# Kernel optimization log

Hardware: AMD Instinct MI355X
Metric: run time of the kernel (lower is better)

Reference implementation:

```python
import jax, jax.numpy as jnp
import numpy as np

B, P, C, D, H = 32, 2048, 19, 512, 4
DH = D // H  # 128
EPS = 1e-5


def setup_inputs() -> dict:
    key = jax.random.key(0)
    ks = jax.random.split(key, 12)
    s = 0.02
    return {
        "x": jax.random.normal(ks[0], (B, P, D), jnp.float32),
        "channel_embeddings": jax.random.normal(ks[1], (C, D), jnp.float32),
        "Wq": jax.random.normal(ks[2], (D, D), jnp.float32) * s,
        "bq": jnp.zeros((D,), jnp.float32),
        "Wk": jax.random.normal(ks[3], (D, D), jnp.float32) * s,
        "bk": jnp.zeros((D,), jnp.float32),
        "Wv": jax.random.normal(ks[4], (D, D), jnp.float32) * s,
        "bv": jnp.zeros((D,), jnp.float32),
        "Wo": jax.random.normal(ks[5], (D, D), jnp.float32) * s,
        "bo": jnp.zeros((D,), jnp.float32),
        "gamma": jnp.ones((D,), jnp.float32),
        "beta": jnp.zeros((D,), jnp.float32),
    }


def reference(x, channel_embeddings, Wq, bq, Wk, bk, Wv, bv, Wo, bo, gamma, beta):
    # q: (B, P, H, DH)
    q = (x @ Wq.T + bq).reshape(B, P, H, DH)
    # K/V depend only on channel embeddings (same for every batch/patch in the
    # original; it merely materialized the broadcast). Compute once: (C, H, DH)
    k = (channel_embeddings @ Wk.T + bk).reshape(C, H, DH)
    v = (channel_embeddings @ Wv.T + bv).reshape(C, H, DH)
    # scores over channels: (B, P, C, H)
    scores = jnp.einsum("bphd,chd->bpch", q, k) / jnp.sqrt(jnp.float32(DH))
    weights = jax.nn.softmax(scores, axis=2)  # softmax over channel dim
    # weighted sum of channel values: (B, P, H, DH) -> (B, P, D)
    attended = jnp.einsum("bpch,chd->bphd", weights, v).reshape(B, P, D)
    out = attended @ Wo.T + bo  # dropout is identity in eval mode
    # residual + layernorm
    h = x + out
    mean = jnp.mean(h, axis=-1, keepdims=True)
    var = jnp.mean(jnp.square(h - mean), axis=-1, keepdims=True)
    return (h - mean) * jax.lax.rsqrt(var + EPS) * gamma + beta
```

## Files before the change

### kernel.cpp

```cpp
#include <hip/hip_runtime.h>
#include <hip/hip_bf16.h>

#define B_  32
#define P_  2048
#define C_  19
#define D_  512
#define H_  4
#define DH_ 128
#define NROW (B_*P_)
#define CHP_ 96

typedef float f32x4 __attribute__((ext_vector_type(4)));
typedef short bf16x8 __attribute__((ext_vector_type(8)));
typedef unsigned short ushort4v __attribute__((ext_vector_type(4)));

__device__ __forceinline__ unsigned short f2bf(float f) {
  union { __hip_bfloat16 h; unsigned short s; } u;
  u.h = __float2bfloat16(f);
  return u.s;
}

__device__ __forceinline__ bf16x8 ld_cvt8(const float* p) {
  f32x4 v0 = *(const f32x4*)p;
  f32x4 v1 = *(const f32x4*)(p + 4);
  bf16x8 a;
  a[0]=(short)f2bf(v0[0]); a[1]=(short)f2bf(v0[1]);
  a[2]=(short)f2bf(v0[2]); a[3]=(short)f2bf(v0[3]);
  a[4]=(short)f2bf(v1[0]); a[5]=(short)f2bf(v1[1]);
  a[6]=(short)f2bf(v1[2]); a[7]=(short)f2bf(v1[3]);
  return a;
}

__global__ __launch_bounds__(256) void prep1(
    const float* __restrict__ ce,
    const float* __restrict__ Wk, const float* __restrict__ bk,
    const float* __restrict__ Wv, const float* __restrict__ bv,
    float* __restrict__ Kg, float* __restrict__ Vg)
{
  int g = blockIdx.x * 256 + threadIdx.x;
  if (g >= 2*C_*D_) return;
  int which = (g >= C_*D_) ? 1 : 0;
  int idx = which ? (g - C_*D_) : g;
  int c = idx >> 9;
  int n = idx & (D_-1);
  const float* w = (which ? Wv : Wk) + (size_t)n * D_;
  const float* e = ce + (size_t)c * D_;
  float s = 0.f;
  #pragma unroll 8
  for (int d = 0; d < D_; ++d) s = fmaf(e[d], w[d], s);
  s += (which ? bv : bk)[n];
  if (which) Vg[idx] = s; else Kg[idx] = s;
}

__global__ __launch_bounds__(512) void prep2(
    const float* __restrict__ Wq, const float* __restrict__ bq,
    const float* __restrict__ Wo,
    const float* __restrict__ Kg, const float* __restrict__ Vg,
    unsigned short* __restrict__ Mtf, unsigned short* __restrict__ Utf,
    float* __restrict__ s0g)
{
  int p = blockIdx.x;
  int m = threadIdx.x;

  const int mt_off = (p>>4)*8192 + (m>>5)*512 + ((((m>>3)&3)<<4) + (p&15))*8 + (m&7);
  const int ut_off = ((m>>4)*3 + (p>>5))*512 + ((((p>>3)&3)<<4) + (m&15))*8 + (p&7);

  int c = p >> 2, h = p & 3;
  if (c >= C_) {
    if (p < 80) { Mtf[mt_off] = 0; if (m == 0) s0g[p] = 0.f; }
    Utf[ut_off] = 0;
    return;
  }
  const float rs128 = 0.08838834764831843f;
  const float* Kr = Kg + c*D_ + h*DH_;
  const float* Vr = Vg + c*D_ + h*DH_;

  float macc = 0.f;
  #pragma unroll 4
  for (int dh = 0; dh < DH_; ++dh)
    macc = fmaf(Wq[(size_t)(h*DH_+dh)*D_ + m], Kr[dh], macc);
  Mtf[mt_off] = f2bf(macc * rs128);

  float uacc = 0.f;
  const float* wor = Wo + (size_t)m*D_ + h*DH_;
  #pragma unroll 4
  for (int dh = 0; dh < DH_; ++dh)
    uacc = fmaf(wor[dh], Vr[dh], uacc);
  Utf[ut_off] = f2bf(uacc);

  if (m == 0) {
    float sa = 0.f;
    const float* bqr = bq + h*DH_;
    for (int dh = 0; dh < DH_; ++dh) sa = fmaf(bqr[dh], Kr[dh], sa);
    s0g[p] = sa * rs128;
  }
}

__global__ __launch_bounds__(256) void fused64(
    const float* __restrict__ x,
    const unsigned short* __restrict__ Mtf,
    const unsigned short* __restrict__ Utf,
    const float* __restrict__ s0g,
    const float* __restrict__ bo,
    const float* __restrict__ gamma, const float* __restrict__ beta,
    float* __restrict__ out)
{
  __shared__ __attribute__((aligned(16))) unsigned short WaL[64][104];
  __shared__ float rs_[64][2], rq_[64][2];

  const int t    = threadIdx.x;
  const int wave = t >> 6;
  const int lane = t & 63;
  const int lhi  = lane >> 4;
  const int llo  = lane & 15;
  const int row0 = blockIdx.x * 64;

  {
    const int wrow = wave * 16;
    f32x4 acc0 = (f32x4){0,0,0,0}, acc1 = acc0, acc2 = acc0, acc3 = acc0, acc4 = acc0;
    const float* xr = x + (size_t)(row0 + wrow + llo)*D_ + lhi*8;
    #pragma unroll
    for (int ks = 0; ks < 16; ++ks) {
      bf16x8 a = ld_cvt8(xr + ks*32);
      acc0 = __builtin_amdgcn_mfma_f32_16x16x32_bf16(a, *(const bf16x8*)(Mtf + 0*8192 + ks*512 + lane*8), acc0, 0, 0, 0);
      acc1 = __builtin_amdgcn_mfma_f32_16x16x32_bf16(a, *(const bf16x8*)(Mtf + 1*8192 + ks*512 + lane*8), acc1, 0, 0, 0);
      acc2 = __builtin_amdgcn_mfma_f32_16x16x32_bf16(a, *(const bf16x8*)(Mtf + 2*8192 + ks*512 + lane*8), acc2, 0, 0, 0);
      acc3 = __builtin_amdgcn_mfma_f32_16x16x32_bf16(a, *(const bf16x8*)(Mtf + 3*8192 + ks*512 + lane*8), acc3, 0, 0, 0);
      acc4 = __builtin_amdgcn_mfma_f32_16x16x32_bf16(a, *(const bf16x8*)(Mtf + 4*8192 + ks*512 + lane*8), acc4, 0, 0, 0);
    }
    const bool dead = (llo >= 12);
    float s0v0 = s0g[llo], s0v1 = s0g[16+llo], s0v2 = s0g[32+llo],
          s0v3 = s0g[48+llo], s0v4 = s0g[64+llo];
    #pragma unroll
    for (int r = 0; r < 4; ++r) {
      float v0 = acc0[r] + s0v0;
      float v1 = acc1[r] + s0v1;
      float v2 = acc2[r] + s0v2;
      float v3 = acc3[r] + s0v3;
      float v4 = dead ? -1e30f : (acc4[r] + s0v4);
      float mx = fmaxf(fmaxf(fmaxf(v0, v1), fmaxf(v2, v3)), v4);
      mx = fmaxf(mx, __shfl_xor(mx, 4, 64));
      mx = fmaxf(mx, __shfl_xor(mx, 8, 64));
      float e0 = __expf(v0 - mx), e1 = __expf(v1 - mx), e2 = __expf(v2 - mx),
            e3 = __expf(v3 - mx), e4 = dead ? 0.f : __expf(v4 - mx);
      float sm = e0 + e1 + e2 + e3 + e4;
      sm += __shfl_xor(sm, 4, 64);
      sm += __shfl_xor(sm, 8, 64);
      float inv = 1.f / sm;
      int lr = wrow + lhi*4 + r;
      WaL[lr][     llo] = f2bf(e0 * inv);
      WaL[lr][16 + llo] = f2bf(e1 * inv);
      WaL[lr][32 + llo] = f2bf(e2 * inv);
      WaL[lr][48 + llo] = f2bf(e3 * inv);
      WaL[lr][64 + llo] = f2bf(e4 * inv);
    }
    *(ushort4v*)&WaL[wrow + lhi*4 + (llo & 3)][80 + (llo >> 2)*4] = (ushort4v){0,0,0,0};
  }
  __syncthreads();

  const int rg = wave >> 1;
  const int cs = wave & 1;
  #pragma unroll
  for (int ha = 0; ha < 2; ++ha) {
    const int hrow = ha * 32;
    f32x4 oacc[16];
    #pragma unroll
    for (int i = 0; i < 16; ++i) oacc[i] = (f32x4){0.f,0.f,0.f,0.f};
    #pragma unroll
    for (int ks = 0; ks < 3; ++ks) {
      bf16x8 a = *(const bf16x8*)&WaL[hrow + rg*16 + llo][ks*32 + lhi*8];
      #pragma unroll
      for (int tile = 0; tile < 16; ++tile) {
        int ntile = cs*16 + tile;
        bf16x8 b = *(const bf16x8*)(Utf + (size_t)(ntile*3 + ks)*512 + lane*8);
        oacc[tile] = __builtin_amdgcn_mfma_f32_16x16x32_bf16(a, b, oacc[tile], 0, 0, 0);
      }
    }

    float s[4] = {0,0,0,0}, q[4] = {0,0,0,0};
    #pragma unroll
    for (int tile = 0; tile < 16; ++tile) {
      int n = cs*256 + tile*16 + llo;
      float bov = bo[n];
      #pragma unroll
      for (int r = 0; r < 4; ++r) {
        int m = hrow + rg*16 + lhi*4 + r;
        float val = oacc[tile][r] + bov + x[(size_t)(row0 + m)*D_ + n];
        oacc[tile][r] = val;
        s[r] += val;
        q[r] = fmaf(val, val, q[r]);
      }
    }
    #pragma unroll
    for (int r = 0; r < 4; ++r) {
      #pragma unroll
      for (int off = 1; off < 16; off <<= 1) {
        s[r] += __shfl_xor(s[r], off, 64);
        q[r] += __shfl_xor(q[r], off, 64);
      }
    }
    if (llo == 0) {
      #pragma unroll
      for (int r = 0; r < 4; ++r) {
        rs_[hrow + rg*16 + lhi*4 + r][cs] = s[r];
        rq_[hrow + rg*16 + lhi*4 + r][cs] = q[r];
      }
    }
    __syncthreads();
    float mu_r[4], rstd_r[4];
    #pragma unroll
    for (int r = 0; r < 4; ++r) {
      int m = hrow + rg*16 + lhi*4 + r;
      float sum = rs_[m][0] + rs_[m][1];
      float sq  = rq_[m][0] + rq_[m][1];
      float mu  = sum * (1.f/(float)D_);
      float var = sq * (1.f/(float)D_) - mu*mu;
      mu_r[r]   = mu;
      rstd_r[r] = rsqrtf(var + 1e-5f);
    }
    #pragma unroll
    for (int tile = 0; tile < 16; ++tile) {
      int n = cs*256 + tile*16 + llo;
      float g = gamma[n], bt = beta[n];
      #pragma unroll
      for (int r = 0; r < 4; ++r) {
        int m = hrow + rg*16 + lhi*4 + r;
        out[(size_t)(row0 + m)*D_ + n] = (oacc[tile][r] - mu_r[r]) * rstd_r[r] * g + bt;
      }
    }
  }
}

extern "C" void kernel_launch(void* const* d_in, const int* in_sizes, int n_in,
                              void* d_out, int out_size, void* d_ws, size_t ws_size,
                              hipStream_t stream) {
  const float* x     = (const float*)d_in[0];
  const float* ce    = (const float*)d_in[1];
  const float* Wq    = (const float*)d_in[2];
  const float* bq    = (const float*)d_in[3];
  const float* Wk    = (const float*)d_in[4];
  const float* bk    = (const float*)d_in[5];
  const float* Wv    = (const float*)d_in[6];
  const float* bv    = (const float*)d_in[7];
  const float* Wo    = (const float*)d_in[8];
  const float* bo    = (const float*)d_in[9];
  const float* gamma = (const float*)d_in[10];
  const float* beta  = (const float*)d_in[11];
  float* out = (float*)d_out;

  char* ws = (char*)d_ws;
  float* Kg           = (float*)(ws);
  float* Vg           = (float*)(ws + 40960);
  unsigned short* Mtf = (unsigned short*)(ws + 81920);
  unsigned short* Utf = (unsigned short*)(ws + 163840);
  float* s0g          = (float*)(ws + 262144);

  prep1<<<(2*C_*D_)/256, 256, 0, stream>>>(ce, Wk, bk, Wv, bv, Kg, Vg);
  prep2<<<CHP_, 512, 0, stream>>>(Wq, bq, Wo, Kg, Vg, Mtf, Utf, s0g);
  fused64<<<NROW/64, 256, 0, stream>>>(x, Mtf, Utf, s0g, bo, gamma, beta, out);
}
```

Before: 139.9 us.

## Shrink fused kernel to 16-row blocks with per-wave redundant softmax scores

The fused kernel now runs 128-thread blocks over 16 rows instead of 256-thread blocks over 64 rows. Each of the two waves recomputes the full score GEMM and softmax for the same 16 rows into its own LDS buffer. That lets the block drop the __syncthreads between the softmax and output-GEMM stages and use a wave-local waitcnt instead. Each wave then handles half of the output columns for the LayerNorm epilogue. The aim is higher occupancy and less block-level synchronisation, at the price of duplicated score MFMAs and repeated reads of x.

```diff
diff --git a/kernel.cpp b/kernel.cpp
--- a/kernel.cpp
+++ b/kernel.cpp
@@ -96,7 +96,7 @@
   }
 }
 
-__global__ __launch_bounds__(256) void fused64(
+__global__ __launch_bounds__(128, 4) void fused16(
     const float* __restrict__ x,
     const unsigned short* __restrict__ Mtf,
     const unsigned short* __restrict__ Utf,
@@ -105,21 +105,20 @@
     const float* __restrict__ gamma, const float* __restrict__ beta,
     float* __restrict__ out)
 {
-  __shared__ __attribute__((aligned(16))) unsigned short WaL[64][104];
-  __shared__ float rs_[64][2], rq_[64][2];
+  __shared__ __attribute__((aligned(16))) unsigned short WaL[2][16][104];
+  __shared__ float rs_[16][2], rq_[16][2];
 
   const int t    = threadIdx.x;
-  const int wave = t >> 6;
+  const int wv   = t >> 6;
   const int lane = t & 63;
   const int lhi  = lane >> 4;
   const int llo  = lane & 15;
-  const int row0 = blockIdx.x * 64;
+  const int row0 = blockIdx.x * 16;
 
   {
-    const int wrow = wave * 16;
     f32x4 acc0 = (f32x4){0,0,0,0}, acc1 = acc0, acc2 = acc0, acc3 = acc0, acc4 = acc0;
-    const float* xr = x + (size_t)(row0 + wrow + llo)*D_ + lhi*8;
-    #pragma unroll
+    const float* xr = x + (size_t)(row0 + llo)*D_ + lhi*8;
+    #pragma unroll 4
     for (int ks = 0; ks < 16; ++ks) {
       bf16x8 a = ld_cvt8(xr + ks*32);
       acc0 = __builtin_amdgcn_mfma_f32_16x16x32_bf16(a, *(const bf16x8*)(Mtf + 0*8192 + ks*512 + lane*8), acc0, 0, 0, 0);
@@ -147,86 +146,81 @@
       sm += __shfl_xor(sm, 4, 64);
       sm += __shfl_xor(sm, 8, 64);
       float inv = 1.f / sm;
-      int lr = wrow + lhi*4 + r;
-      WaL[lr][     llo] = f2bf(e0 * inv);
-      WaL[lr][16 + llo] = f2bf(e1 * inv);
-      WaL[lr][32 + llo] = f2bf(e2 * inv);
-      WaL[lr][48 + llo] = f2bf(e3 * inv);
-      WaL[lr][64 + llo] = f2bf(e4 * inv);
-    }
-    *(ushort4v*)&WaL[wrow + lhi*4 + (llo & 3)][80 + (llo >> 2)*4] = (ushort4v){0,0,0,0};
+      int lr = lhi*4 + r;
+      WaL[wv][lr][     llo] = f2bf(e0 * inv);
+      WaL[wv][lr][16 + llo] = f2bf(e1 * inv);
+      WaL[wv][lr][32 + llo] = f2bf(e2 * inv);
+      WaL[wv][lr][48 + llo] = f2bf(e3 * inv);
+      WaL[wv][lr][64 + llo] = f2bf(e4 * inv);
+    }
+    *(ushort4v*)&WaL[wv][lane & 15][80 + (lane >> 4)*4] = (ushort4v){0,0,0,0};
+  }
+  asm volatile("s_waitcnt lgkmcnt(0)" ::: "memory");
+  __builtin_amdgcn_sched_barrier(0);
+
+  f32x4 oacc[16];
+  #pragma unroll
+  for (int i = 0; i < 16; ++i) oacc[i] = (f32x4){0.f,0.f,0.f,0.f};
+  #pragma unroll
+  for (int ks = 0; ks < 3; ++ks) {
+    bf16x8 a = *(const bf16x8*)&WaL[wv][llo][ks*32 + lhi*8];
+    #pragma unroll
+    for (int tile = 0; tile < 16; ++tile) {
+      int ntile = wv*16 + tile;
+      bf16x8 b = *(const bf16x8*)(Utf + (size_t)(ntile*3 + ks)*512 + lane*8);
+      oacc[tile] = __builtin_amdgcn_mfma_f32_16x16x32_bf16(a, b, oacc[tile], 0, 0, 0);
+    }
+  }
+
+  float s[4] = {0,0,0,0}, q[4] = {0,0,0,0};
+  #pragma unroll
+  for (int tile = 0; tile < 16; ++tile) {
+    int n = wv*256 + tile*16 + llo;
+    float bov = bo[n];
+    #pragma unroll
+    for (int r = 0; r < 4; ++r) {
+      int m = lhi*4 + r;
+      float val = oacc[tile][r] + bov + x[(size_t)(row0 + m)*D_ + n];
+      oacc[tile][r] = val;
+      s[r] += val;
+      q[r] = fmaf(val, val, q[r]);
+    }
+  }
+  #pragma unroll
+  for (int r = 0; r < 4; ++r) {
+    #pragma unroll
+    for (int off = 1; off < 16; off <<= 1) {
+      s[r] += __shfl_xor(s[r], off, 64);
+      q[r] += __shfl_xor(q[r], off, 64);
+    }
+  }
+  if (llo == 0) {
+    #pragma unroll
+    for (int r = 0; r < 4; ++r) {
+      rs_[lhi*4 + r][wv] = s[r];
+      rq_[lhi*4 + r][wv] = q[r];
+    }
   }
   __syncthreads();
-
-  const int rg = wave >> 1;
-  const int cs = wave & 1;
-  #pragma unroll
-  for (int ha = 0; ha < 2; ++ha) {
-    const int hrow = ha * 32;
-    f32x4 oacc[16];
-    #pragma unroll
-    for (int i = 0; i < 16; ++i) oacc[i] = (f32x4){0.f,0.f,0.f,0.f};
-    #pragma unroll
-    for (int ks = 0; ks < 3; ++ks) {
-      bf16x8 a = *(const bf16x8*)&WaL[hrow + rg*16 + llo][ks*32 + lhi*8];
-      #pragma unroll
-      for (int tile = 0; tile < 16; ++tile) {
-        int ntile = cs*16 + tile;
-        bf16x8 b = *(const bf16x8*)(Utf + (size_t)(ntile*3 + ks)*512 + lane*8);
-        oacc[tile] = __builtin_amdgcn_mfma_f32_16x16x32_bf16(a, b, oacc[tile], 0, 0, 0);
-      }
-    }
-
-    float s[4] = {0,0,0,0}, q[4] = {0,0,0,0};
-    #pragma unroll
-    for (int tile = 0; tile < 16; ++tile) {
-      int n = cs*256 + tile*16 + llo;
-      float bov = bo[n];
-      #pragma unroll
-      for (int r = 0; r < 4; ++r) {
-        int m = hrow + rg*16 + lhi*4 + r;
-        float val = oacc[tile][r] + bov + x[(size_t)(row0 + m)*D_ + n];
-        oacc[tile][r] = val;
-        s[r] += val;
-        q[r] = fmaf(val, val, q[r]);
-      }
-    }
-    #pragma unroll
-    for (int r = 0; r < 4; ++r) {
-      #pragma unroll
-      for (int off = 1; off < 16; off <<= 1) {
-        s[r] += __shfl_xor(s[r], off, 64);
-        q[r] += __shfl_xor(q[r], off, 64);
-      }
-    }
-    if (llo == 0) {
-      #pragma unroll
-      for (int r = 0; r < 4; ++r) {
-        rs_[hrow + rg*16 + lhi*4 + r][cs] = s[r];
-        rq_[hrow + rg*16 + lhi*4 + r][cs] = q[r];
-      }
-    }
-    __syncthreads();
-    float mu_r[4], rstd_r[4];
-    #pragma unroll
-    for (int r = 0; r < 4; ++r) {
-      int m = hrow + rg*16 + lhi*4 + r;
-      float sum = rs_[m][0] + rs_[m][1];
-      float sq  = rq_[m][0] + rq_[m][1];
-      float mu  = sum * (1.f/(float)D_);
-      float var = sq * (1.f/(float)D_) - mu*mu;
-      mu_r[r]   = mu;
-      rstd_r[r] = rsqrtf(var + 1e-5f);
-    }
-    #pragma unroll
-    for (int tile = 0; tile < 16; ++tile) {
-      int n = cs*256 + tile*16 + llo;
-      float g = gamma[n], bt = beta[n];
-      #pragma unroll
-      for (int r = 0; r < 4; ++r) {
-        int m = hrow + rg*16 + lhi*4 + r;
-        out[(size_t)(row0 + m)*D_ + n] = (oacc[tile][r] - mu_r[r]) * rstd_r[r] * g + bt;
-      }
+  float mu_r[4], rstd_r[4];
+  #pragma unroll
+  for (int r = 0; r < 4; ++r) {
+    int m = lhi*4 + r;
+    float sum = rs_[m][0] + rs_[m][1];
+    float sq  = rq_[m][0] + rq_[m][1];
+    float mu  = sum * (1.f/(float)D_);
+    float var = sq * (1.f/(float)D_) - mu*mu;
+    mu_r[r]   = mu;
+    rstd_r[r] = rsqrtf(var + 1e-5f);
+  }
+  #pragma unroll
+  for (int tile = 0; tile < 16; ++tile) {
+    int n = wv*256 + tile*16 + llo;
+    float g = gamma[n], bt = beta[n];
+    #pragma unroll
+    for (int r = 0; r < 4; ++r) {
+      int m = lhi*4 + r;
+      out[(size_t)(row0 + m)*D_ + n] = (oacc[tile][r] - mu_r[r]) * rstd_r[r] * g + bt;
     }
   }
 }
@@ -257,5 +251,5 @@
 
   prep1<<<(2*C_*D_)/256, 256, 0, stream>>>(ce, Wk, bk, Wv, bv, Kg, Vg);
   prep2<<<CHP_, 512, 0, stream>>>(Wq, bq, Wo, Kg, Vg, Mtf, Utf, s0g);
-  fused64<<<NROW/64, 256, 0, stream>>>(x, Mtf, Utf, s0g, bo, gamma, beta, out);
-}
+  fused16<<<NROW/16, 128, 0, stream>>>(x, Mtf, Utf, s0g, bo, gamma, beta, out);
+}
```

New measurement: 174.5 us. 24.7% more time.
